# Optimization experiments

Hardware: AMD Instinct MI355X
Metric: run time of the kernel (lower is better)

Reference implementation:

```python
import jax, jax.numpy as jnp
import numpy as np
import math

KV_STRIDE = 2
Q_STRIDE = 1
WAVE_LEN = 1000.0
POS_MAG = 1.0


def _pos_embed(h, w, h_kv, w_kv, q_stride, kv_stride, feat_dim):
    # Sinusoidal relative-position embeddings, matching get_position_embedding.
    h_idx = jnp.arange(h, dtype=jnp.float32) * q_stride
    w_idx = jnp.arange(w, dtype=jnp.float32) * q_stride
    h_kv_idx = jnp.arange(h_kv, dtype=jnp.float32) * kv_stride
    w_kv_idx = jnp.arange(w_kv, dtype=jnp.float32) * kv_stride
    h_diff = (h_idx[:, None] - h_kv_idx[None, :]) * POS_MAG  # (h, h_kv)
    w_diff = (w_idx[:, None] - w_kv_idx[None, :]) * POS_MAG  # (w, w_kv)
    feat_range = jnp.arange(feat_dim // 4, dtype=jnp.float32)
    dim_mat = WAVE_LEN ** (4.0 / feat_dim * feat_range)  # (feat_dim//4,)
    wd = w_diff[:, :, None] / dim_mat  # (w, w_kv, F)
    hd = h_diff[:, :, None] / dim_mat  # (h, h_kv, F)
    emb_x = jnp.concatenate([jnp.sin(wd), jnp.cos(wd)], axis=2)  # (w, w_kv, feat_dim//2)
    emb_y = jnp.concatenate([jnp.sin(hd), jnp.cos(hd)], axis=2)  # (h, h_kv, feat_dim//2)
    return emb_x, emb_y


def setup_inputs() -> dict:
    key = jax.random.key(0)
    ks = jax.random.split(key, 11)
    C = 288
    s = 1.0 / math.sqrt(C)
    return {
        'x_input': jax.random.normal(ks[0], (2, C, 64, 64), jnp.float32),
        'Wq': jax.random.normal(ks[1], (C, C), jnp.float32) * s,
        'Wk': jax.random.normal(ks[2], (C, C), jnp.float32) * s,
        'Wv': jax.random.normal(ks[3], (C, C), jnp.float32) * s,
        'Wx': jax.random.normal(ks[4], (C, C // 2), jnp.float32) * s,
        'Wy': jax.random.normal(ks[5], (C, C // 2), jnp.float32) * s,
        'Wproj': jax.random.normal(ks[6], (C, C), jnp.float32) * s,
        'bproj': jax.random.normal(ks[7], (C,), jnp.float32) * 0.02,
        'Wc': jax.random.normal(ks[8], (9, C), jnp.float32) * s,
        'bc': jax.random.normal(ks[9], (9,), jnp.float32) * 0.02,
        'gamma': jax.random.normal(ks[10], (1,), jnp.float32),
    }


def reference(x_input, Wq, Wk, Wv, Wx, Wy, Wproj, bproj, Wc, bc, gamma):
    M = Wc.shape[0]                       # num_mixtures
    n, C, h, w = x_input.shape
    d = Wq.shape[0] // M                  # qk_embed_dim (== v_dim)
    x_q = x_input                         # q_stride == 1
    x_kv = x_input[:, :, ::KV_STRIDE, ::KV_STRIDE]  # AvgPool2d(k=1, stride=2)
    h_kv, w_kv = x_kv.shape[2], x_kv.shape[3]

    # 1x1 convs as channel GEMMs
    q = jnp.einsum('nchw,oc->nohw', x_q, Wq).reshape(n, M, d, h * w)
    q = q.transpose(0, 1, 3, 2)                                    # (n,M,hw,d)
    k = jnp.einsum('nchw,oc->nohw', x_kv, Wk).reshape(n, M, d, h_kv * w_kv)

    emb_x, emb_y = _pos_embed(h, w, h_kv, w_kv, Q_STRIDE, KV_STRIDE, C)
    inv_sqrt2 = 1.0 / math.sqrt(2.0)
    pf_x = (emb_x @ Wx.T).reshape(w, w_kv, M, d).transpose(2, 0, 1, 3) * inv_sqrt2  # (M,w,w_kv,d)
    pf_y = (emb_y @ Wy.T).reshape(h, h_kv, M, d).transpose(2, 0, 1, 3) * inv_sqrt2  # (M,h,h_kv,d)

    energy = jnp.matmul(q, k).reshape(n, M, h, w, h_kv, w_kv)
    q5 = q.reshape(n, M, h, w, d)
    e_x = jnp.einsum('nmhwd,mwvd->nmhwv', q5, pf_x)  # (n,M,h,w,w_kv)
    e_y = jnp.einsum('nmhwd,mhud->nmhwu', q5, pf_y)  # (n,M,h,w,h_kv)
    energy = energy + e_x[:, :, :, :, None, :] + e_y[:, :, :, :, :, None]
    energy = energy.reshape(n, M, h * w, h_kv * w_kv)
    attn = jax.nn.softmax(energy, axis=3)

    # Learned per-mixture gating from mean query context
    context = q.transpose(0, 1, 3, 2).reshape(n, M * d, h * w).mean(axis=2)  # (n, M*d)
    mix_w = jax.nn.softmax(context @ Wc.T + bc, axis=1)                      # (n, M)
    attn = jnp.sum(attn * mix_w[:, :, None, None], axis=1)                   # (n,hw,hw_kv)

    v = jnp.einsum('nchw,oc->nohw', x_kv, Wv).reshape(n, M * d, h_kv * w_kv)
    v = v.transpose(0, 2, 1)                                                 # (n,hw_kv,M*d)
    out = jnp.matmul(attn, v).transpose(0, 2, 1).reshape(n, M * d, h, w)
    out = jnp.einsum('nchw,oc->nohw', out, Wproj) + bproj[None, :, None, None]
    return gamma[0] * out + x_input
```

## Files before the change

kernel.cpp:

```cpp
#include <hip/hip_runtime.h>
#include <math.h>

#define NB     2
#define CDIM   288
#define HW     4096
#define PKV    1024
#define MHEAD  9
#define DHEAD  32

typedef __attribute__((ext_vector_type(8))) short bf16x8;
typedef __attribute__((ext_vector_type(4))) float f32x4;

__device__ inline unsigned short f2bf(float x) {
    unsigned int u = __float_as_uint(x);
    u = (u + 0x7fffu + ((u >> 16) & 1u)) >> 16;
    return (unsigned short)u;
}


__global__ __launch_bounds__(256) void prep(const float* __restrict__ X,
        const float* __restrict__ Wq, const float* __restrict__ Wk,
        const float* __restrict__ Wv, const float* __restrict__ Wproj,
        const float* __restrict__ Wx, const float* __restrict__ Wy,
        unsigned short* __restrict__ XF, unsigned short* __restrict__ WFq,
        unsigned short* __restrict__ WFk, unsigned short* __restrict__ WFv,
        unsigned short* __restrict__ WFp, float* __restrict__ WTx,
        float* __restrict__ WTy, float* __restrict__ MX) {
    __shared__ float t32[32][33];
    __shared__ float t16[16][17];
    __shared__ float red[4];
    int b = blockIdx.x;
    int tid = threadIdx.x;
    if (b < 2304) {
        int bx = b % 128, by = (b / 128) % 9, n = b / 1152;
        int j0 = bx * 32, c0 = by * 32;
        int tx = tid & 31, ty = tid >> 5;
#pragma unroll
        for (int l = 0; l < 4; ++l) {
            int c = ty + l * 8;
            t32[c][tx] = X[((size_t)n * CDIM + c0 + c) * HW + j0 + tx];
        }
        __syncthreads();
        int s = tid >> 7;
        int u = tid & 127;
        int lane = u >> 1, e0 = (u & 1) * 4;
        int jl = s * 16 + (lane & 15);
        int cb = (lane >> 4) * 8 + e0;
        unsigned int w0 = f2bf(t32[cb + 0][jl]) | ((unsigned int)f2bf(t32[cb + 1][jl]) << 16);
        unsigned int w1 = f2bf(t32[cb + 2][jl]) | ((unsigned int)f2bf(t32[cb + 3][jl]) << 16);
        int jt = (j0 >> 4) + s, cc = c0 >> 5;
        unsigned short* O = XF + (size_t)n * HW * CDIM + ((size_t)jt * 9 + cc) * 512 + lane * 8 + e0;
        uint2 pk = { w0, w1 };
        *(uint2*)O = pk;
    } else if (b < 2628) {
        int u = b - 2304;
        int bx = u % 9, by = (u / 9) % 18, bz = u / 162;
        const float* W = bz ? Wy : Wx;
        float* WT      = bz ? WTy : WTx;
        int f0 = bx * 16, o0 = by * 16;
        int tx = tid & 15, ty = tid >> 4;
        t16[ty][tx] = W[(o0 + ty) * 144 + f0 + tx];
        __syncthreads();
        WT[(f0 + ty) * 288 + o0 + tx] = t16[tx][ty];
    } else if (b < 2790) {
        int t = b - 2628;
        int sub = tid >> 6, lane = tid & 63;
        int ot = t / 9, cc = t % 9;
        const float* W = (sub == 0) ? Wq : (sub == 1) ? Wk : (sub == 2) ? Wv : Wproj;
        unsigned short* O = ((sub == 0) ? WFq : (sub == 1) ? WFk : (sub == 2) ? WFv : WFp)
                            + (size_t)t * 512;
        int o  = ot * 16 + (lane & 15);
        int c0 = cc * 32 + (lane >> 4) * 8;
        const float* src = W + (size_t)o * CDIM + c0;
        float4 f0 = *(const float4*)src, f1 = *(const float4*)(src + 4);
        unsigned int v0 = f2bf(f0.x) | ((unsigned int)f2bf(f0.y) << 16);
        unsigned int v1 = f2bf(f0.z) | ((unsigned int)f2bf(f0.w) << 16);
        unsigned int v2 = f2bf(f1.x) | ((unsigned int)f2bf(f1.y) << 16);
        unsigned int v3 = f2bf(f1.z) | ((unsigned int)f2bf(f1.w) << 16);
        uint4 pk = { v0, v1, v2, v3 };
        *(uint4*)(O + lane * 8) = pk;
    } else {
        int bid = b - 2790;
        const float* xr = X + (size_t)bid * HW;
        float s = 0.f;
        for (int j = tid; j < HW; j += 256) s += xr[j];
        for (int off = 32; off > 0; off >>= 1) s += __shfl_xor(s, off, 64);
        if ((tid & 63) == 0) red[tid >> 6] = s;
        __syncthreads();
        if (tid == 0) MX[bid] = (red[0] + red[1] + red[2] + red[3]) * (1.f / 4096.f);
    }
}

__global__ __launch_bounds__(256) void mid(
        const float* __restrict__ WTx, const float* __restrict__ WTy,
        unsigned short* __restrict__ FXb, unsigned short* __restrict__ FYb,
        const float* __restrict__ Wq, const float* __restrict__ MX,
        const float* __restrict__ Wc, const float* __restrict__ bc,
        float* __restrict__ MIXW,
        const unsigned short* __restrict__ WFq, const unsigned short* __restrict__ WFk,
        const unsigned short* __restrict__ WFv, const unsigned short* __restrict__ XF,
        unsigned short* __restrict__ Qf, unsigned short* __restrict__ KF,
        unsigned short* __restrict__ VF) {
    __shared__ float emb[144];
    __shared__ float ctx_s[NB * CDIM];
    __shared__ float lg[18];
    __shared__ __attribute__((aligned(16))) unsigned short tr[4][32][40];
    int b = blockIdx.x;
    int tid = threadIdx.x;

    if (b < 252) {
        int axis = b / 126;
        int dif  = b % 126;
        float diff = (float)(dif - 62);
        if (tid < 72) {
            float dm = expf(6.9077552789821368f * ((float)tid * (1.f / 72.f)));
            float t  = diff / dm;
            emb[tid]      = sinf(t);
            emb[72 + tid] = cosf(t);
        }
        __syncthreads();
        const float* WT = axis ? WTy : WTx;
        unsigned short* F = axis ? FYb : FXb;
        for (int o = tid; o < CDIM; o += 256) {
            float s = 0.f;
#pragma unroll 8
            for (int f = 0; f < 144; ++f) s += emb[f] * WT[f * 288 + o];
            int m = o >> 5, d = o & 31;
            F[(size_t)(m * 8 + (dif >> 4)) * 512 + ((dif & 15) + 16 * (d >> 3)) * 8 + (d & 7)]
                = f2bf(s * 0.70710678118654752f);
        }
    } else if (b == 252) {
        for (int idx = tid; idx < 1152; idx += 256) {
            int d = idx & 31, rr = (idx >> 5) & 1, mm = (idx >> 6) % 9, ax = idx / 576;
            int dif = 126 + rr;
            unsigned short* F = ax ? FYb : FXb;
            F[(size_t)(mm * 8 + 7) * 512 + ((dif & 15) + 16 * (d >> 3)) * 8 + (d & 7)] = 0;
        }
        for (int p = tid; p < NB * CDIM; p += 256) {
            int n = p / CDIM, o = p % CDIM;
            const float* wr = Wq + (size_t)o * CDIM;
            const float* mx = MX + n * CDIM;
            float s = 0.f;
            for (int c = 0; c < CDIM; c += 4) {
                float4 w4 = *(const float4*)&wr[c];
                float4 m4 = *(const float4*)&mx[c];
                s += w4.x * m4.x + w4.y * m4.y + w4.z * m4.z + w4.w * m4.w;
            }
            ctx_s[p] = s;
        }
        __syncthreads();
        if (tid < 18) {
            int n = tid / 9, j = tid % 9;
            float s = bc[j];
            for (int o = 0; o < CDIM; ++o) s += ctx_s[n * CDIM + o] * Wc[j * CDIM + o];
            lg[tid] = s;
        }
        __syncthreads();
        if (tid < 2) {
            float mx = -1e30f;
            for (int j = 0; j < 9; ++j) mx = fmaxf(mx, lg[tid * 9 + j]);
            float e[9], sm = 0.f;
            for (int j = 0; j < 9; ++j) { e[j] = __expf(lg[tid * 9 + j] - mx); sm += e[j]; }
            for (int j = 0; j < 9; ++j) MIXW[tid * 9 + j] = e[j] / sm;
        }
    } else {
        int bx = b - 253;
        int gx = bx % 40;
        int m  = (bx / 40) % 9;
        int n  = bx / 360;
        int wv = tid >> 6, lane = tid & 63;
        int lq = lane & 15, quad = lane >> 4;
        if (gx < 32) {
            int j0 = gx * 128;
            int jw = j0 + wv * 32;
            const unsigned short* Wb = WFq + ((size_t)(m * 2) * 9) * 512 + lane * 8;
            const unsigned short* Xb = XF + (size_t)n * HW * CDIM + ((size_t)(jw >> 4) * 9) * 512 + lane * 8;
            f32x4 acc[2][2] = {};
#pragma unroll
            for (int cc = 0; cc < 9; ++cc) {
                bf16x8 a0 = *(const bf16x8*)(Wb + (size_t)cc * 512);
                bf16x8 a1 = *(const bf16x8*)(Wb + (size_t)(9 + cc) * 512);
                bf16x8 b0 = *(const bf16x8*)(Xb + (size_t)cc * 512);
                bf16x8 b1 = *(const bf16x8*)(Xb + (size_t)(9 + cc) * 512);
                acc[0][0] = __builtin_amdgcn_mfma_f32_16x16x32_bf16(a0, b0, acc[0][0], 0, 0, 0);
                acc[0][1] = __builtin_amdgcn_mfma_f32_16x16x32_bf16(a0, b1, acc[0][1], 0, 0, 0);
                acc[1][0] = __builtin_amdgcn_mfma_f32_16x16x32_bf16(a1, b0, acc[1][0], 0, 0, 0);
                acc[1][1] = __builtin_amdgcn_mfma_f32_16x16x32_bf16(a1, b1, acc[1][1], 0, 0, 0);
            }
#pragma unroll
            for (int oi = 0; oi < 2; ++oi)
#pragma unroll
                for (int ji = 0; ji < 2; ++ji)
#pragma unroll
                    for (int r = 0; r < 4; ++r)
                        tr[wv][ji * 16 + lq][oi * 16 + quad * 4 + r] = f2bf(acc[oi][ji][r]);
            int jl = lane & 31, half = lane >> 5;
            bf16x8 v0 = *(const bf16x8*)&tr[wv][jl][half * 16];
            bf16x8 v1 = *(const bf16x8*)&tr[wv][jl][half * 16 + 8];
            unsigned short* Qm = Qf + ((size_t)(n * MHEAD + m) * HW + jw + jl) * 32 + half * 16;
            *(bf16x8*)Qm = v0;
            *(bf16x8*)(Qm + 8) = v1;
        } else {
            int p0 = (gx - 32) * 128;
            int pw = p0 + wv * 32;
            const unsigned short* XFn = XF + (size_t)n * HW * CDIM;
            size_t bidx[2];
#pragma unroll
            for (int pi = 0; pi < 2; ++pi) {
                int p   = pw + pi * 16 + lq;
                int pos = ((p >> 5) << 7) + ((p & 31) << 1);
                bidx[pi] = ((size_t)(pos >> 4) * 9) * 512 + ((pos & 15) + 16 * quad) * 8;
            }
            const unsigned short* Wkb = WFk + ((size_t)(m * 2) * 9) * 512 + lane * 8;
            const unsigned short* Wvb = WFv + ((size_t)(m * 2) * 9) * 512 + lane * 8;
            f32x4 ak[2][2] = {}, av[2][2] = {};
#pragma unroll
            for (int cc = 0; cc < 9; ++cc) {
                bf16x8 a0k = *(const bf16x8*)(Wkb + (size_t)cc * 512);
                bf16x8 a1k = *(const bf16x8*)(Wkb + (size_t)(9 + cc) * 512);
                bf16x8 a0v = *(const bf16x8*)(Wvb + (size_t)cc * 512);
                bf16x8 a1v = *(const bf16x8*)(Wvb + (size_t)(9 + cc) * 512);
                bf16x8 b0  = *(const bf16x8*)(XFn + bidx[0] + (size_t)cc * 512);
                bf16x8 b1  = *(const bf16x8*)(XFn + bidx[1] + (size_t)cc * 512);
                ak[0][0] = __builtin_amdgcn_mfma_f32_16x16x32_bf16(a0k, b0, ak[0][0], 0, 0, 0);
                ak[0][1] = __builtin_amdgcn_mfma_f32_16x16x32_bf16(a0k, b1, ak[0][1], 0, 0, 0);
                ak[1][0] = __builtin_amdgcn_mfma_f32_16x16x32_bf16(a1k, b0, ak[1][0], 0, 0, 0);
                ak[1][1] = __builtin_amdgcn_mfma_f32_16x16x32_bf16(a1k, b1, ak[1][1], 0, 0, 0);
                av[0][0] = __builtin_amdgcn_mfma_f32_16x16x32_bf16(a0v, b0, av[0][0], 0, 0, 0);
                av[0][1] = __builtin_amdgcn_mfma_f32_16x16x32_bf16(a0v, b1, av[0][1], 0, 0, 0);
                av[1][0] = __builtin_amdgcn_mfma_f32_16x16x32_bf16(a1v, b0, av[1][0], 0, 0, 0);
                av[1][1] = __builtin_amdgcn_mfma_f32_16x16x32_bf16(a1v, b1, av[1][1], 0, 0, 0);
            }
#pragma unroll
            for (int oi = 0; oi < 2; ++oi)
#pragma unroll
                for (int pi = 0; pi < 2; ++pi)
#pragma unroll
                    for (int r = 0; r < 4; ++r)
                        tr[wv][pi * 16 + lq][oi * 16 + quad * 4 + r] = f2bf(ak[oi][pi][r]);
            unsigned short* KFm = KF + (size_t)(n * MHEAD + m) * (PKV * 32);
#pragma unroll
            for (int pi = 0; pi < 2; ++pi) {
                bf16x8 v = *(const bf16x8*)&tr[wv][pi * 16 + lq][quad * 8];
                *(bf16x8*)(KFm + (size_t)((pw >> 4) + pi) * 512 + lane * 8) = v;
            }
#pragma unroll
            for (int oi = 0; oi < 2; ++oi)
#pragma unroll
                for (int pi = 0; pi < 2; ++pi)
#pragma unroll
                    for (int r = 0; r < 4; ++r)
                        tr[wv][oi * 16 + quad * 4 + r][pi * 16 + lq] = f2bf(av[oi][pi][r]);
            unsigned short* VFn = VF + (size_t)n * CDIM * PKV;
#pragma unroll
            for (int oi = 0; oi < 2; ++oi) {
                bf16x8 v = *(const bf16x8*)&tr[wv][oi * 16 + lq][quad * 8];
                *(bf16x8*)(VFn + (size_t)((m * 2 + oi) * 32 + (pw >> 5)) * 512 + lane * 8) = v;
            }
        }
    }
}

__global__ __launch_bounds__(512, 4) void attn_fused2(
        const unsigned short* __restrict__ Qf, const unsigned short* __restrict__ KF,
        const unsigned short* __restrict__ VF, const unsigned short* __restrict__ WFp,
        const unsigned short* __restrict__ FXb, const unsigned short* __restrict__ FYb,
        const float* __restrict__ MIXW, const float* __restrict__ bproj,
        const float* __restrict__ x, const float* __restrict__ gamma,
        float* __restrict__ OUT) {
    int n    = blockIdx.x >> 8;
    int i0   = (blockIdx.x & 255) * 16;
    int tid  = threadIdx.x;
    int wv   = tid >> 6;
    int lane = tid & 63;
    int lq   = lane & 15;
    int quad = lane >> 4;

    int bx_t = (i0 & 63) >> 4;
    int h    = i0 >> 6;
    int by_t = h >> 4;
    int dh   = h & 15;

    __shared__ float Rx_s[16][82];
    __shared__ float Ry_s[16][82];
    __shared__ float ws_s[8][16];
    __shared__ __attribute__((aligned(16))) unsigned short tr[16][1032];
    __shared__ __attribute__((aligned(16))) unsigned short Mt[16][296];

    float mixed[8][4];
#pragma unroll
    for (int t = 0; t < 8; ++t)
#pragma unroll
        for (int j = 0; j < 4; ++j) mixed[t][j] = 0.f;

    for (int m = 0; m < MHEAD; ++m) {
        const unsigned short* Qm  = Qf + ((size_t)(n * MHEAD + m) * HW + i0) * 32;
        const unsigned short* KmF = KF + (size_t)(n * MHEAD + m) * (PKV * 32);
        bf16x8 afrag = *(const bf16x8*)(Qm + (size_t)lq * 32 + quad * 8);

        if (wv < 5) {
            bf16x8 bR = *(const bf16x8*)(FXb + (size_t)(m * 8 + bx_t + wv) * 512 + lane * 8);
            f32x4 r = (f32x4){0.f, 0.f, 0.f, 0.f};
            r = __builtin_amdgcn_mfma_f32_16x16x32_bf16(afrag, bR, r, 0, 0, 0);
#pragma unroll
            for (int reg = 0; reg < 4; ++reg)
                Rx_s[quad * 4 + reg][wv * 16 + lq] = r[reg];
        } else {
            bf16x8 bR = *(const bf16x8*)(FYb + (size_t)(m * 8 + by_t + (wv - 5)) * 512 + lane * 8);
            f32x4 r = (f32x4){0.f, 0.f, 0.f, 0.f};
            r = __builtin_amdgcn_mfma_f32_16x16x32_bf16(afrag, bR, r, 0, 0, 0);
#pragma unroll
            for (int reg = 0; reg < 4; ++reg)
                Ry_s[quad * 4 + reg][(wv - 5) * 16 + lq] = r[reg];
        }
        if (wv < 2) {
            bf16x8 bR = *(const bf16x8*)(FYb + (size_t)(m * 8 + by_t + 3 + wv) * 512 + lane * 8);
            f32x4 r = (f32x4){0.f, 0.f, 0.f, 0.f};
            r = __builtin_amdgcn_mfma_f32_16x16x32_bf16(afrag, bR, r, 0, 0, 0);
#pragma unroll
            for (int reg = 0; reg < 4; ++reg)
                Ry_s[quad * 4 + reg][(3 + wv) * 16 + lq] = r[reg];
        }
        __syncthreads();

        bf16x8 bf[8];
#pragma unroll
        for (int t = 0; t < 8; ++t)
            bf[t] = *(const bf16x8*)(KmF + (size_t)(wv * 8 + t) * 512 + lane * 8);
        f32x4 acc[8];
#pragma unroll
        for (int t = 0; t < 8; ++t) acc[t] = (f32x4){0.f, 0.f, 0.f, 0.f};
#pragma unroll
        for (int t = 0; t < 8; ++t)
            acc[t] = __builtin_amdgcn_mfma_f32_16x16x32_bf16(afrag, bf[t], acc[t], 0, 0, 0);

        float exA[4], exB[4];
#pragma unroll
        for (int j = 0; j < 4; ++j) {
            int q = quad * 4 + j;
            exA[j] = Rx_s[q][q + 62 - 2 * lq];
            exB[j] = Rx_s[q][q + 30 - 2 * lq];
        }

        float rs[4] = {0.f, 0.f, 0.f, 0.f};
#pragma unroll
        for (int tp = 0; tp < 4; ++tp) {
            int u = wv * 4 + tp;
            float ey[4];
#pragma unroll
            for (int j = 0; j < 4; ++j) ey[j] = Ry_s[quad * 4 + j][dh + 62 - 2 * u];
#pragma unroll
            for (int half = 0; half < 2; ++half) {
                int t = tp * 2 + half;
#pragma unroll
                for (int j = 0; j < 4; ++j) {
                    float e = __expf(acc[t][j] + (half ? exB[j] : exA[j]) + ey[j]);
                    rs[j] += e;
                    acc[t][j] = e;
                }
            }
        }
#pragma unroll
        for (int j = 0; j < 4; ++j) {
            rs[j] += __shfl_xor(rs[j], 1, 64);
            rs[j] += __shfl_xor(rs[j], 2, 64);
            rs[j] += __shfl_xor(rs[j], 4, 64);
            rs[j] += __shfl_xor(rs[j], 8, 64);
        }
        if (lq == 0) {
#pragma unroll
            for (int j = 0; j < 4; ++j) ws_s[wv][quad * 4 + j] = rs[j];
        }
        __syncthreads();

        float wm = MIXW[n * MHEAD + m];
#pragma unroll
        for (int j = 0; j < 4; ++j) {
            int q = quad * 4 + j;
            float lt = 0.f;
#pragma unroll
            for (int w = 0; w < 8; ++w) lt += ws_s[w][q];
            float fct = wm / lt;
#pragma unroll
            for (int t = 0; t < 8; ++t) mixed[t][j] += acc[t][j] * fct;
        }
    }

#pragma unroll
    for (int t = 0; t < 8; ++t)
#pragma unroll
        for (int j = 0; j < 4; ++j)
            tr[quad * 4 + j][wv * 128 + t * 16 + lq] = f2bf(mixed[t][j]);
    __syncthreads();

    const unsigned short* VFn = VF + (size_t)n * CDIM * PKV;
    f32x4 accpv[3];
#pragma unroll
    for (int idx = 0; idx < 3; ++idx) accpv[idx] = (f32x4){0.f, 0.f, 0.f, 0.f};
#pragma unroll 4
    for (int pc = 0; pc < 32; ++pc) {
        bf16x8 pf = *(const bf16x8*)&tr[lq][pc * 32 + quad * 8];
#pragma unroll
        for (int idx = 0; idx < 3; ++idx) {
            int ot = wv + idx * 8;
            if (ot < 18) {
                bf16x8 vf = *(const bf16x8*)(VFn + (size_t)(ot * 32 + pc) * 512 + lane * 8);
                accpv[idx] = __builtin_amdgcn_mfma_f32_16x16x32_bf16(pf, vf, accpv[idx], 0, 0, 0);
            }
        }
    }
#pragma unroll
    for (int idx = 0; idx < 3; ++idx) {
        int ot = wv + idx * 8;
        if (ot < 18) {
#pragma unroll
            for (int r = 0; r < 4; ++r)
                Mt[quad * 4 + r][ot * 16 + lq] = f2bf(accpv[idx][r]);
        }
    }
    __syncthreads();

    float g = gamma[0];
#pragma unroll
    for (int idx = 0; idx < 3; ++idx) {
        int ot = wv + idx * 8;
        if (ot >= 18) continue;
        f32x4 acc = (f32x4){0.f, 0.f, 0.f, 0.f};
#pragma unroll
        for (int cc = 0; cc < 9; ++cc) {
            bf16x8 af = *(const bf16x8*)(WFp + (size_t)(ot * 9 + cc) * 512 + lane * 8);
            bf16x8 bfm = *(const bf16x8*)&Mt[lq][cc * 32 + quad * 8];
            acc = __builtin_amdgcn_mfma_f32_16x16x32_bf16(af, bfm, acc, 0, 0, 0);
        }
#pragma unroll
        for (int r = 0; r < 4; ++r) {
            int o = ot * 16 + quad * 4 + r;
            size_t id = ((size_t)(n * CDIM) + o) * HW + i0 + lq;
            OUT[id] = g * (acc[r] + bproj[o]) + x[id];
        }
    }
}

extern "C" void kernel_launch(void* const* d_in, const int* in_sizes, int n_in,
                              void* d_out, int out_size, void* d_ws, size_t ws_size,
                              hipStream_t stream) {
    const float* x     = (const float*)d_in[0];
    const float* Wq    = (const float*)d_in[1];
    const float* Wk    = (const float*)d_in[2];
    const float* Wv    = (const float*)d_in[3];
    const float* Wx    = (const float*)d_in[4];
    const float* Wy    = (const float*)d_in[5];
    const float* Wproj = (const float*)d_in[6];
    const float* bproj = (const float*)d_in[7];
    const float* Wc    = (const float*)d_in[8];
    const float* bc    = (const float*)d_in[9];
    const float* gamma = (const float*)d_in[10];
    float* out = (float*)d_out;

    float* ws = (float*)d_ws;
    size_t off = 0;
    unsigned short* Qf  = (unsigned short*)(ws + off); off += (size_t)NB * MHEAD * HW * 32 / 2;
    unsigned short* KF  = (unsigned short*)(ws + off); off += (size_t)NB * MHEAD * PKV * 32 / 2;
    unsigned short* VF  = (unsigned short*)(ws + off); off += (size_t)NB * CDIM * PKV / 2;
    unsigned short* WFq = (unsigned short*)(ws + off); off += (size_t)CDIM * CDIM / 2;
    unsigned short* WFk = (unsigned short*)(ws + off); off += (size_t)CDIM * CDIM / 2;
    unsigned short* WFv = (unsigned short*)(ws + off); off += (size_t)CDIM * CDIM / 2;
    unsigned short* WFp = (unsigned short*)(ws + off); off += (size_t)CDIM * CDIM / 2;
    unsigned short* XF  = (unsigned short*)(ws + off); off += (size_t)NB * HW * CDIM / 2;
    float* WTx  = ws + off; off += 144 * 288;
    float* WTy  = ws + off; off += 144 * 288;
    unsigned short* FXb = (unsigned short*)(ws + off); off += (size_t)MHEAD * 8 * 512 / 2;
    unsigned short* FYb = (unsigned short*)(ws + off); off += (size_t)MHEAD * 8 * 512 / 2;
    float* MX   = ws + off; off += NB * CDIM;
    float* MIXW = ws + off; off += 32;

    prep<<<3366, 256, 0, stream>>>(x, Wq, Wk, Wv, Wproj, Wx, Wy,
                                   XF, WFq, WFk, WFv, WFp, WTx, WTy, MX);
    mid<<<973, 256, 0, stream>>>(WTx, WTy, FXb, FYb, Wq, MX, Wc, bc, MIXW,
                                 WFq, WFk, WFv, XF, Qf, KF, VF);
    attn_fused2<<<NB * HW / 16, 512, 0, stream>>>(Qf, KF, VF, WFp, FXb, FYb, MIXW,
                                                  bproj, x, gamma, out);
}
```

Measured before the change: 178.6 us.

## Double-buffer position-bias tiles across heads and widen prep transpose tiles

The attention kernel now computes the relative-position bias tiles for head m+1 into a second shared buffer while head m is processed. This removes one block-wide barrier per head and overlaps the bias MFMAs with the QK work. The prep kernel now transposes 128-column tiles with float4 loads, cutting its block count. The cost is more shared memory (larger t32, two R buffers) and more live registers for the prefetched Q fragment, which could lower occupancy.

```diff
diff --git a/kernel.cpp b/kernel.cpp
--- a/kernel.cpp
+++ b/kernel.cpp
@@ -26,34 +26,40 @@
         unsigned short* __restrict__ WFk, unsigned short* __restrict__ WFv,
         unsigned short* __restrict__ WFp, float* __restrict__ WTx,
         float* __restrict__ WTy, float* __restrict__ MX) {
-    __shared__ float t32[32][33];
+    __shared__ float t32[32][133];
     __shared__ float t16[16][17];
     __shared__ float red[4];
     int b = blockIdx.x;
     int tid = threadIdx.x;
-    if (b < 2304) {
-        int bx = b % 128, by = (b / 128) % 9, n = b / 1152;
-        int j0 = bx * 32, c0 = by * 32;
-        int tx = tid & 31, ty = tid >> 5;
+    if (b < 576) {
+        int bx = b % 32, by = (b / 32) % 9, n = b / 288;
+        int j0 = bx * 128, c0 = by * 32;
+        int c = tid >> 3, f = tid & 7;
+        const float* src = &X[((size_t)n * CDIM + c0 + c) * HW + j0];
 #pragma unroll
         for (int l = 0; l < 4; ++l) {
-            int c = ty + l * 8;
-            t32[c][tx] = X[((size_t)n * CDIM + c0 + c) * HW + j0 + tx];
-        }
-        __syncthreads();
-        int s = tid >> 7;
-        int u = tid & 127;
-        int lane = u >> 1, e0 = (u & 1) * 4;
-        int jl = s * 16 + (lane & 15);
-        int cb = (lane >> 4) * 8 + e0;
-        unsigned int w0 = f2bf(t32[cb + 0][jl]) | ((unsigned int)f2bf(t32[cb + 1][jl]) << 16);
-        unsigned int w1 = f2bf(t32[cb + 2][jl]) | ((unsigned int)f2bf(t32[cb + 3][jl]) << 16);
-        int jt = (j0 >> 4) + s, cc = c0 >> 5;
-        unsigned short* O = XF + (size_t)n * HW * CDIM + ((size_t)jt * 9 + cc) * 512 + lane * 8 + e0;
-        uint2 pk = { w0, w1 };
-        *(uint2*)O = pk;
-    } else if (b < 2628) {
-        int u = b - 2304;
+            float4 v = *(const float4*)&src[(f + l * 8) * 4];
+            *(float4*)&t32[c][(f + l * 8) * 4] = v;
+        }
+        __syncthreads();
+        int cc = c0 >> 5;
+#pragma unroll
+        for (int l = 0; l < 4; ++l) {
+            int g = l * 256 + tid;
+            int s = g >> 7;
+            int w = g & 127;
+            int lane = w >> 1, e0 = (w & 1) * 4;
+            int jl = s * 16 + (lane & 15);
+            int cb = (lane >> 4) * 8 + e0;
+            unsigned int w0 = f2bf(t32[cb + 0][jl]) | ((unsigned int)f2bf(t32[cb + 1][jl]) << 16);
+            unsigned int w1 = f2bf(t32[cb + 2][jl]) | ((unsigned int)f2bf(t32[cb + 3][jl]) << 16);
+            int jt = (j0 >> 4) + s;
+            unsigned short* O = XF + (size_t)n * HW * CDIM + ((size_t)jt * 9 + cc) * 512 + lane * 8 + e0;
+            uint2 pk = { w0, w1 };
+            *(uint2*)O = pk;
+        }
+    } else if (b < 900) {
+        int u = b - 576;
         int bx = u % 9, by = (u / 9) % 18, bz = u / 162;
         const float* W = bz ? Wy : Wx;
         float* WT      = bz ? WTy : WTx;
@@ -62,8 +68,8 @@
         t16[ty][tx] = W[(o0 + ty) * 144 + f0 + tx];
         __syncthreads();
         WT[(f0 + ty) * 288 + o0 + tx] = t16[tx][ty];
-    } else if (b < 2790) {
-        int t = b - 2628;
+    } else if (b < 1062) {
+        int t = b - 900;
         int sub = tid >> 6, lane = tid & 63;
         int ot = t / 9, cc = t % 9;
         const float* W = (sub == 0) ? Wq : (sub == 1) ? Wk : (sub == 2) ? Wv : Wproj;
@@ -80,7 +86,7 @@
         uint4 pk = { v0, v1, v2, v3 };
         *(uint4*)(O + lane * 8) = pk;
     } else {
-        int bid = b - 2790;
+        int bid = b - 1062;
         const float* xr = X + (size_t)bid * HW;
         float s = 0.f;
         for (int j = tid; j < HW; j += 256) s += xr[j];
@@ -261,7 +267,7 @@
     }
 }
 
-__global__ __launch_bounds__(512, 4) void attn_fused2(
+__global__ __launch_bounds__(512, 4) void attn_fused3(
         const unsigned short* __restrict__ Qf, const unsigned short* __restrict__ KF,
         const unsigned short* __restrict__ VF, const unsigned short* __restrict__ WFp,
         const unsigned short* __restrict__ FXb, const unsigned short* __restrict__ FYb,
@@ -281,9 +287,8 @@
     int by_t = h >> 4;
     int dh   = h & 15;
 
-    __shared__ float Rx_s[16][82];
-    __shared__ float Ry_s[16][82];
-    __shared__ float ws_s[8][16];
+    __shared__ float R_s[2][2][16][84];
+    __shared__ float ws_s[2][8][16];
     __shared__ __attribute__((aligned(16))) unsigned short tr[16][1032];
     __shared__ __attribute__((aligned(16))) unsigned short Mt[16][296];
 
@@ -293,53 +298,64 @@
 #pragma unroll
         for (int j = 0; j < 4; ++j) mixed[t][j] = 0.f;
 
+    auto computeR = [&](bf16x8 af, int mh, int bufn) {
+        if (wv < 5) {
+            bf16x8 bR = *(const bf16x8*)(FXb + (size_t)(mh * 8 + bx_t + wv) * 512 + lane * 8);
+            f32x4 r = (f32x4){0.f, 0.f, 0.f, 0.f};
+            r = __builtin_amdgcn_mfma_f32_16x16x32_bf16(af, bR, r, 0, 0, 0);
+#pragma unroll
+            for (int reg = 0; reg < 4; ++reg)
+                R_s[bufn][0][quad * 4 + reg][wv * 16 + lq] = r[reg];
+        } else {
+            bf16x8 bR = *(const bf16x8*)(FYb + (size_t)(mh * 8 + by_t + (wv - 5)) * 512 + lane * 8);
+            f32x4 r = (f32x4){0.f, 0.f, 0.f, 0.f};
+            r = __builtin_amdgcn_mfma_f32_16x16x32_bf16(af, bR, r, 0, 0, 0);
+#pragma unroll
+            for (int reg = 0; reg < 4; ++reg)
+                R_s[bufn][1][quad * 4 + reg][(wv - 5) * 16 + lq] = r[reg];
+        }
+        if (wv < 2) {
+            bf16x8 bR = *(const bf16x8*)(FYb + (size_t)(mh * 8 + by_t + 3 + wv) * 512 + lane * 8);
+            f32x4 r = (f32x4){0.f, 0.f, 0.f, 0.f};
+            r = __builtin_amdgcn_mfma_f32_16x16x32_bf16(af, bR, r, 0, 0, 0);
+#pragma unroll
+            for (int reg = 0; reg < 4; ++reg)
+                R_s[bufn][1][quad * 4 + reg][(3 + wv) * 16 + lq] = r[reg];
+        }
+    };
+
+    bf16x8 afrag = *(const bf16x8*)(Qf + ((size_t)(n * MHEAD) * HW + i0 + lq) * 32 + quad * 8);
+    computeR(afrag, 0, 0);
+    __syncthreads();
+
     for (int m = 0; m < MHEAD; ++m) {
-        const unsigned short* Qm  = Qf + ((size_t)(n * MHEAD + m) * HW + i0) * 32;
+        int buf = m & 1;
         const unsigned short* KmF = KF + (size_t)(n * MHEAD + m) * (PKV * 32);
-        bf16x8 afrag = *(const bf16x8*)(Qm + (size_t)lq * 32 + quad * 8);
-
-        if (wv < 5) {
-            bf16x8 bR = *(const bf16x8*)(FXb + (size_t)(m * 8 + bx_t + wv) * 512 + lane * 8);
-            f32x4 r = (f32x4){0.f, 0.f, 0.f, 0.f};
-            r = __builtin_amdgcn_mfma_f32_16x16x32_bf16(afrag, bR, r, 0, 0, 0);
-#pragma unroll
-            for (int reg = 0; reg < 4; ++reg)
-                Rx_s[quad * 4 + reg][wv * 16 + lq] = r[reg];
-        } else {
-            bf16x8 bR = *(const bf16x8*)(FYb + (size_t)(m * 8 + by_t + (wv - 5)) * 512 + lane * 8);
-            f32x4 r = (f32x4){0.f, 0.f, 0.f, 0.f};
-            r = __builtin_amdgcn_mfma_f32_16x16x32_bf16(afrag, bR, r, 0, 0, 0);
-#pragma unroll
-            for (int reg = 0; reg < 4; ++reg)
-                Ry_s[quad * 4 + reg][(wv - 5) * 16 + lq] = r[reg];
-        }
-        if (wv < 2) {
-            bf16x8 bR = *(const bf16x8*)(FYb + (size_t)(m * 8 + by_t + 3 + wv) * 512 + lane * 8);
-            f32x4 r = (f32x4){0.f, 0.f, 0.f, 0.f};
-            r = __builtin_amdgcn_mfma_f32_16x16x32_bf16(afrag, bR, r, 0, 0, 0);
-#pragma unroll
-            for (int reg = 0; reg < 4; ++reg)
-                Ry_s[quad * 4 + reg][(3 + wv) * 16 + lq] = r[reg];
-        }
-        __syncthreads();
-
-        bf16x8 bf[8];
+
+        bf16x8 kf[8];
 #pragma unroll
         for (int t = 0; t < 8; ++t)
-            bf[t] = *(const bf16x8*)(KmF + (size_t)(wv * 8 + t) * 512 + lane * 8);
+            kf[t] = *(const bf16x8*)(KmF + (size_t)(wv * 8 + t) * 512 + lane * 8);
+
+        bf16x8 afragN = afrag;
+        if (m < MHEAD - 1) {
+            afragN = *(const bf16x8*)(Qf + ((size_t)(n * MHEAD + m + 1) * HW + i0 + lq) * 32 + quad * 8);
+            computeR(afragN, m + 1, buf ^ 1);
+        }
+
         f32x4 acc[8];
 #pragma unroll
         for (int t = 0; t < 8; ++t) acc[t] = (f32x4){0.f, 0.f, 0.f, 0.f};
 #pragma unroll
         for (int t = 0; t < 8; ++t)
-            acc[t] = __builtin_amdgcn_mfma_f32_16x16x32_bf16(afrag, bf[t], acc[t], 0, 0, 0);
+            acc[t] = __builtin_amdgcn_mfma_f32_16x16x32_bf16(afrag, kf[t], acc[t], 0, 0, 0);
 
         float exA[4], exB[4];
 #pragma unroll
         for (int j = 0; j < 4; ++j) {
             int q = quad * 4 + j;
-            exA[j] = Rx_s[q][q + 62 - 2 * lq];
-            exB[j] = Rx_s[q][q + 30 - 2 * lq];
+            exA[j] = R_s[buf][0][q][q + 62 - 2 * lq];
+            exB[j] = R_s[buf][0][q][q + 30 - 2 * lq];
         }
 
         float rs[4] = {0.f, 0.f, 0.f, 0.f};
@@ -348,7 +364,7 @@
             int u = wv * 4 + tp;
             float ey[4];
 #pragma unroll
-            for (int j = 0; j < 4; ++j) ey[j] = Ry_s[quad * 4 + j][dh + 62 - 2 * u];
+            for (int j = 0; j < 4; ++j) ey[j] = R_s[buf][1][quad * 4 + j][dh + 62 - 2 * u];
 #pragma unroll
             for (int half = 0; half < 2; ++half) {
                 int t = tp * 2 + half;
@@ -369,7 +385,7 @@
         }
         if (lq == 0) {
 #pragma unroll
-            for (int j = 0; j < 4; ++j) ws_s[wv][quad * 4 + j] = rs[j];
+            for (int j = 0; j < 4; ++j) ws_s[buf][wv][quad * 4 + j] = rs[j];
         }
         __syncthreads();
 
@@ -379,11 +395,12 @@
             int q = quad * 4 + j;
             float lt = 0.f;
 #pragma unroll
-            for (int w = 0; w < 8; ++w) lt += ws_s[w][q];
+            for (int w = 0; w < 8; ++w) lt += ws_s[buf][w][q];
             float fct = wm / lt;
 #pragma unroll
             for (int t = 0; t < 8; ++t) mixed[t][j] += acc[t][j] * fct;
         }
+        afrag = afragN;
     }
 
 #pragma unroll
@@ -474,10 +491,10 @@
     float* MX   = ws + off; off += NB * CDIM;
     float* MIXW = ws + off; off += 32;
 
-    prep<<<3366, 256, 0, stream>>>(x, Wq, Wk, Wv, Wproj, Wx, Wy,
+    prep<<<1638, 256, 0, stream>>>(x, Wq, Wk, Wv, Wproj, Wx, Wy,
                                    XF, WFq, WFk, WFv, WFp, WTx, WTy, MX);
     mid<<<973, 256, 0, stream>>>(WTx, WTy, FXb, FYb, Wq, MX, Wc, bc, MIXW,
                                  WFq, WFk, WFv, XF, Qf, KF, VF);
-    attn_fused2<<<NB * HW / 16, 512, 0, stream>>>(Qf, KF, VF, WFp, FXb, FYb, MIXW,
+    attn_fused3<<<NB * HW / 16, 512, 0, stream>>>(Qf, KF, VF, WFp, FXb, FYb, MIXW,
                                                   bproj, x, gamma, out);
 }
```

Result: slower. 188.3 us (+5.5%).
